# Kernel optimization log

Hardware: AMD Instinct MI355X
Metric: run time of the kernel (lower is better)

The kernel has to match this reference:

```python
import jax, jax.numpy as jnp
import numpy as np

N_NODES = 100_000
N_EDGES = 1_600_000
N_GRAPHS = 64
IN_CH = 128
HID = 64
OUT_CH = 2


def setup_inputs() -> dict:
    key = jax.random.key(0)
    ks = jax.random.split(key, 12)

    def lin(k, fan_in, fan_out):
        s = 1.0 / np.sqrt(fan_in)
        return jax.random.uniform(k, (fan_in, fan_out), jnp.float32, -s, s)

    x = jax.random.normal(ks[0], (N_NODES, IN_CH), jnp.float32)
    edge_index = jax.random.randint(ks[1], (2, N_EDGES), 0, N_NODES, jnp.int64)
    batch = jnp.sort(jax.random.randint(ks[2], (N_NODES,), 0, N_GRAPHS, jnp.int64))
    return {
        "x": x,
        "edge_index": edge_index,
        "batch": batch,
        "w_rel0": lin(ks[3], IN_CH, HID),
        "b_rel0": jnp.zeros((HID,), jnp.float32),
        "w_root0": lin(ks[4], IN_CH, HID),
        "w_rel1": lin(ks[5], HID, HID),
        "b_rel1": jnp.zeros((HID,), jnp.float32),
        "w_root1": lin(ks[6], HID, HID),
        "w_rel2": lin(ks[7], HID, HID),
        "b_rel2": jnp.zeros((HID,), jnp.float32),
        "w_root2": lin(ks[8], HID, HID),
        "head_w1": lin(ks[9], HID, HID),
        "head_b1": jnp.zeros((HID,), jnp.float32),
        "head_w2": lin(ks[10], HID, OUT_CH),
        "head_b2": jnp.zeros((OUT_CH,), jnp.float32),
    }


def _graph_conv(x, src, dst, w_rel, b_rel, w_root):
    # PyG GraphConv: out = lin_rel(sum_{j->i} x_j) + lin_root(x_i)
    agg = jax.ops.segment_sum(x[src], dst, num_segments=N_NODES)  # [N, d_in]
    return agg @ w_rel + b_rel + x @ w_root


def reference(x, edge_index, batch, w_rel0, b_rel0, w_root0,
              w_rel1, b_rel1, w_root1, w_rel2, b_rel2, w_root2,
              head_w1, head_b1, head_w2, head_b2):
    src, dst = edge_index[0], edge_index[1]
    h = jax.nn.relu(_graph_conv(x, src, dst, w_rel0, b_rel0, w_root0))
    h = jax.nn.relu(_graph_conv(h, src, dst, w_rel1, b_rel1, w_root1))
    h = jax.nn.relu(_graph_conv(h, src, dst, w_rel2, b_rel2, w_root2))
    # global_mean_pool over graph ids (dropout is identity at inference)
    sums = jax.ops.segment_sum(h, batch, num_segments=N_GRAPHS)          # [G, H]
    cnts = jax.ops.segment_sum(jnp.ones((N_NODES,), h.dtype), batch,
                               num_segments=N_GRAPHS)                    # [G]
    pooled = sums / jnp.maximum(cnts, 1.0)[:, None]
    z = jax.nn.relu(pooled @ head_w1 + head_b1)
    return z @ head_w2 + head_b2
```

## Files before the change

kernel.cpp:

```cpp
#include <hip/hip_runtime.h>
#include <hip/hip_bf16.h>

#define CAP 64
#define KBUCK 391
#define BSHIFT 8
#define BCAP 4608
#define CHUNK_A 2048
#define AITER (CHUNK_A / 256)
#define LDSZ 36864

typedef __attribute__((ext_vector_type(8))) short short8;
typedef __attribute__((ext_vector_type(4))) float f32x4;

__device__ inline unsigned short bfbits(float f) {
    __hip_bfloat16 b = __float2bfloat16(f);
    unsigned short u;
    __builtin_memcpy(&u, &b, 2);
    return u;
}

__device__ inline void bucket_body(char* smem, int bb, const int* __restrict__ ei,
                                   int E, int* __restrict__ gcur,
                                   unsigned* __restrict__ bucketed)
{
    int* hist = (int*)smem;
    int* base = hist + KBUCK;
    const int e0 = bb * CHUNK_A;
    const int e1 = min(e0 + CHUNK_A, E);
    for (int i = threadIdx.x; i < KBUCK; i += 256) hist[i] = 0;
    __syncthreads();
    int dreg[AITER];
    #pragma unroll
    for (int it = 0; it < AITER; ++it) {
        int e = e0 + it * 256 + threadIdx.x;
        dreg[it] = (e < e1) ? ei[E + e] : -1;
        if (dreg[it] >= 0) atomicAdd(&hist[dreg[it] >> BSHIFT], 1);
    }
    __syncthreads();
    for (int i = threadIdx.x; i < KBUCK; i += 256) {
        int h = hist[i];
        base[i] = h ? atomicAdd(&gcur[i], h) : 0;
        hist[i] = 0;
    }
    __syncthreads();
    #pragma unroll
    for (int it = 0; it < AITER; ++it) {
        int e = e0 + it * 256 + threadIdx.x;
        if (e < e1) {
            int s = ei[e];
            int d = dreg[it];
            int b = d >> BSHIFT;
            int off = base[b] + atomicAdd(&hist[b], 1);
            if (off < BCAP)
                bucketed[(size_t)b * BCAP + off] = ((unsigned)s << 8) | (unsigned)(d & 255);
        }
    }
}

__global__ __launch_bounds__(256) void build_slots_kernel(
    const unsigned* __restrict__ bucketed, const int* __restrict__ gcur,
    int* __restrict__ cnt, int* __restrict__ slots, int N)
{
    __shared__ int lcnt[256];
    const int b = blockIdx.x;
    const int nb0 = b << BSHIFT;
    lcnt[threadIdx.x] = 0;
    __syncthreads();
    const int count = min(gcur[b], BCAP);
    const unsigned* src = bucketed + (size_t)b * BCAP;
    for (int i = threadIdx.x; i < count; i += 256) {
        unsigned p = src[i];
        int dl = (int)(p & 255u);
        int pos = atomicAdd(&lcnt[dl], 1);
        if (pos < CAP) slots[(size_t)(nb0 + dl) * CAP + pos] = (int)(p >> 8);
    }
    __syncthreads();
    int node = nb0 + threadIdx.x;
    if (node < N) cnt[node] = min(lcnt[threadIdx.x], CAP);
}

__global__ __launch_bounds__(256) void prep_weights_kernel(
    const float* __restrict__ wr0, const float* __restrict__ wt0,
    const float* __restrict__ wr1, const float* __restrict__ wt1,
    const float* __restrict__ wr2, const float* __restrict__ wt2,
    __hip_bfloat16* __restrict__ hi, __hip_bfloat16* __restrict__ lo)
{
    int idx = blockIdx.x * 256 + threadIdx.x;
    if (idx >= 32768) return;
    const float *wr, *wt;
    int n, k;
    if (idx < 16384)      { wr = wr0; wt = wt0; int r = idx;         n = r >> 7; k = r & 127; }
    else if (idx < 24576) { wr = wr1; wt = wt1; int r = idx - 16384; n = r >> 6; k = r & 63; }
    else                  { wr = wr2; wt = wt2; int r = idx - 24576; n = r >> 6; k = r & 63; }
    float w = (n < 64) ? wr[k * 64 + n] : wt[k * 64 + (n - 64)];
    __hip_bfloat16 h = __float2bfloat16(w);
    hi[idx] = h;
    lo[idx] = __float2bfloat16(w - __bfloat162float(h));
}

template <int DIN, bool AFP32>
__device__ inline void mfma_body(
    char* smem, int bx, const void* __restrict__ featv,
    const __hip_bfloat16* __restrict__ whiT, const __hip_bfloat16* __restrict__ wloT,
    const float* __restrict__ b_rel,
    __hip_bfloat16* __restrict__ y, __hip_bfloat16* __restrict__ r, int N)
{
    __hip_bfloat16* As = (__hip_bfloat16*)smem;
    __hip_bfloat16* Bh = As + 128 * 48;
    __hip_bfloat16* Bl = Bh + 128 * 48;
    const int t = threadIdx.x;
    const int lane = t & 63;
    const int wid = t >> 6;
    const int wm = wid >> 1, wn = wid & 1;
    const int node0 = bx * 128;
    const int lrow = lane & 15;
    const int kgrp = lane >> 4;

    f32x4 acc[4][4];
    #pragma unroll
    for (int i = 0; i < 4; ++i)
        #pragma unroll
        for (int j = 0; j < 4; ++j) acc[i][j] = (f32x4){0.f, 0.f, 0.f, 0.f};

    for (int ks = 0; ks < DIN / 32; ++ks) {
        #pragma unroll
        for (int p = 0; p < 2; ++p) {
            int c = t + p * 256;
            int m = c >> 2, kc = c & 3;
            int row = node0 + m; if (row >= N) row = N - 1;
            if (AFP32) {
                const float* feat = (const float*)featv;
                const float* src = feat + (size_t)row * DIN + ks * 32 + kc * 8;
                float4 v0 = *(const float4*)src;
                float4 v1 = *(const float4*)(src + 4);
                union { uint4 q; unsigned short s[8]; } pk;
                pk.s[0] = bfbits(v0.x); pk.s[1] = bfbits(v0.y);
                pk.s[2] = bfbits(v0.z); pk.s[3] = bfbits(v0.w);
                pk.s[4] = bfbits(v1.x); pk.s[5] = bfbits(v1.y);
                pk.s[6] = bfbits(v1.z); pk.s[7] = bfbits(v1.w);
                *(uint4*)&As[m * 48 + kc * 8] = pk.q;
            } else {
                const __hip_bfloat16* feat = (const __hip_bfloat16*)featv;
                *(uint4*)&As[m * 48 + kc * 8] =
                    *(const uint4*)(feat + (size_t)row * DIN + ks * 32 + kc * 8);
            }
        }
        #pragma unroll
        for (int p = 0; p < 4; ++p) {
            int c = t + p * 256;
            int half = c >> 9;
            int cc = c & 511;
            int n = cc >> 2, kc = cc & 3;
            const __hip_bfloat16* w = half ? wloT : whiT;
            uint4 v = *(const uint4*)(w + (size_t)n * DIN + ks * 32 + kc * 8);
            if (half) *(uint4*)&Bl[n * 48 + kc * 8] = v;
            else      *(uint4*)&Bh[n * 48 + kc * 8] = v;
        }
        __syncthreads();

        short8 a[4], bh[4], bl[4];
        #pragma unroll
        for (int i = 0; i < 4; ++i)
            a[i] = *(const short8*)&As[(wm * 64 + i * 16 + lrow) * 48 + kgrp * 8];
        #pragma unroll
        for (int j = 0; j < 4; ++j) {
            bh[j] = *(const short8*)&Bh[(wn * 64 + j * 16 + lrow) * 48 + kgrp * 8];
            bl[j] = *(const short8*)&Bl[(wn * 64 + j * 16 + lrow) * 48 + kgrp * 8];
        }
        #pragma unroll
        for (int i = 0; i < 4; ++i)
            #pragma unroll
            for (int j = 0; j < 4; ++j) {
                acc[i][j] = __builtin_amdgcn_mfma_f32_16x16x32_bf16(a[i], bh[j], acc[i][j], 0, 0, 0);
                acc[i][j] = __builtin_amdgcn_mfma_f32_16x16x32_bf16(a[i], bl[j], acc[i][j], 0, 0, 0);
            }
        __syncthreads();
    }

    #pragma unroll
    for (int i = 0; i < 4; ++i) {
        int mbase = node0 + wm * 64 + i * 16 + kgrp * 4;
        #pragma unroll
        for (int j = 0; j < 4; ++j) {
            int n = wn * 64 + j * 16 + lrow;
            #pragma unroll
            for (int v = 0; v < 4; ++v) {
                int m = mbase + v;
                if (m < N) {
                    float val = acc[i][j][v];
                    if (n < 64) y[(size_t)m * 64 + n] = __float2bfloat16(val);
                    else        r[(size_t)m * 64 + (n - 64)] = __float2bfloat16(val + b_rel[n - 64]);
                }
            }
        }
    }
}

__global__ __launch_bounds__(256) void fused_l0_kernel(
    const float* __restrict__ x,
    const __hip_bfloat16* __restrict__ whiT, const __hip_bfloat16* __restrict__ wloT,
    const float* __restrict__ b_rel,
    __hip_bfloat16* __restrict__ y, __hip_bfloat16* __restrict__ r, int N,
    int gemm_blocks, const int* __restrict__ ei, int E,
    int* __restrict__ gcur, unsigned* __restrict__ bucketed)
{
    extern __shared__ char smem[];
    if ((int)blockIdx.x < gemm_blocks)
        mfma_body<128, true>(smem, blockIdx.x, x, whiT, wloT, b_rel, y, r, N);
    else
        bucket_body(smem, blockIdx.x - gemm_blocks, ei, E, gcur, bucketed);
}

template <int DIN>
__global__ __launch_bounds__(256) void mfma_lin_kernel(
    const __hip_bfloat16* __restrict__ feat,
    const __hip_bfloat16* __restrict__ whiT, const __hip_bfloat16* __restrict__ wloT,
    const float* __restrict__ b_rel,
    __hip_bfloat16* __restrict__ y, __hip_bfloat16* __restrict__ r, int N)
{
    extern __shared__ char smem[];
    mfma_body<DIN, false>(smem, blockIdx.x, feat, whiT, wloT, b_rel, y, r, N);
}

__global__ __launch_bounds__(256) void gather_relu_kernel(
    const __hip_bfloat16* __restrict__ y, const int* __restrict__ cnt,
    const int* __restrict__ slots, const __hip_bfloat16* __restrict__ rin,
    __hip_bfloat16* __restrict__ hout, int N)
{
    const int node = blockIdx.x * 8 + (threadIdx.x >> 5);
    if (node >= N) return;
    const int sub = threadIdx.x & 31;
    const int nb = sub >> 3;
    const int ch = (sub & 7) * 8;
    const int deg = cnt[node];
    const int* sl = slots + (size_t)node * CAP;
    const unsigned short* yp = (const unsigned short*)y;

    float a[8], b[8];
    #pragma unroll
    for (int k = 0; k < 8; ++k) { a[k] = 0.f; b[k] = 0.f; }

    #pragma unroll 2
    for (int j = nb; j < deg; j += 8) {
        int n0 = sl[j];
        uint4 v = *(const uint4*)(yp + (size_t)n0 * 64 + ch);
        a[0] += __uint_as_float(v.x << 16); a[1] += __uint_as_float(v.x & 0xffff0000u);
        a[2] += __uint_as_float(v.y << 16); a[3] += __uint_as_float(v.y & 0xffff0000u);
        a[4] += __uint_as_float(v.z << 16); a[5] += __uint_as_float(v.z & 0xffff0000u);
        a[6] += __uint_as_float(v.w << 16); a[7] += __uint_as_float(v.w & 0xffff0000u);
        int j2 = j + 4;
        if (j2 < deg) {
            int n1 = sl[j2];
            uint4 w = *(const uint4*)(yp + (size_t)n1 * 64 + ch);
            b[0] += __uint_as_float(w.x << 16); b[1] += __uint_as_float(w.x & 0xffff0000u);
            b[2] += __uint_as_float(w.y << 16); b[3] += __uint_as_float(w.y & 0xffff0000u);
            b[4] += __uint_as_float(w.z << 16); b[5] += __uint_as_float(w.z & 0xffff0000u);
            b[6] += __uint_as_float(w.w << 16); b[7] += __uint_as_float(w.w & 0xffff0000u);
        }
    }
    #pragma unroll
    for (int k = 0; k < 8; ++k) {
        a[k] += b[k];
        a[k] += __shfl_xor(a[k], 8);
        a[k] += __shfl_xor(a[k], 16);
    }
    if (nb == 0) {
        uint4 rv = *(const uint4*)((const unsigned short*)rin + (size_t)node * 64 + ch);
        float r0 = __uint_as_float(rv.x << 16), r1 = __uint_as_float(rv.x & 0xffff0000u);
        float r2 = __uint_as_float(rv.y << 16), r3 = __uint_as_float(rv.y & 0xffff0000u);
        float r4 = __uint_as_float(rv.z << 16), r5 = __uint_as_float(rv.z & 0xffff0000u);
        float r6 = __uint_as_float(rv.w << 16), r7 = __uint_as_float(rv.w & 0xffff0000u);
        float f0 = fmaxf(r0 + a[0], 0.f), f1 = fmaxf(r1 + a[1], 0.f);
        float f2 = fmaxf(r2 + a[2], 0.f), f3 = fmaxf(r3 + a[3], 0.f);
        float f4 = fmaxf(r4 + a[4], 0.f), f5 = fmaxf(r5 + a[5], 0.f);
        float f6 = fmaxf(r6 + a[6], 0.f), f7 = fmaxf(r7 + a[7], 0.f);
        union { uint4 q; unsigned short s[8]; } pk;
        pk.s[0] = bfbits(f0); pk.s[1] = bfbits(f1); pk.s[2] = bfbits(f2); pk.s[3] = bfbits(f3);
        pk.s[4] = bfbits(f4); pk.s[5] = bfbits(f5); pk.s[6] = bfbits(f6); pk.s[7] = bfbits(f7);
        *(uint4*)((unsigned short*)hout + (size_t)node * 64 + ch) = pk.q;
    }
}

__global__ __launch_bounds__(256) void pool_kernel(
    const __hip_bfloat16* __restrict__ h, const int* __restrict__ batch,
    float* __restrict__ gsum, int* __restrict__ gcnt, int N)
{
    const int CHUNK = 64;
    int wid = (blockIdx.x * 256 + threadIdx.x) >> 6;
    int lane = threadIdx.x & 63;
    int nb = lane >> 3;
    int ch = (lane & 7) * 8;
    int start = wid * CHUNK;
    if (start >= N) return;
    int end = min(start + CHUNK, N);
    const unsigned short* hp = (const unsigned short*)h;

    float a[8];
    #pragma unroll
    for (int k = 0; k < 8; ++k) a[k] = 0.f;
    int runcnt = 0;
    int i = start;
    int gcur = batch[start];

    while (i < end) {
        int idx = i + lane; if (idx > end - 1) idx = end - 1;
        int bl = batch[idx];
        unsigned long long diff = __ballot(bl != gcur && (i + lane) < end);
        int len = diff ? ((int)__ffsll(diff) - 1) : min(64, end - i);
        for (int j = i + nb; j < i + len; j += 8) {
            uint4 v = *(const uint4*)(hp + (size_t)j * 64 + ch);
            a[0] += __uint_as_float(v.x << 16); a[1] += __uint_as_float(v.x & 0xffff0000u);
            a[2] += __uint_as_float(v.y << 16); a[3] += __uint_as_float(v.y & 0xffff0000u);
            a[4] += __uint_as_float(v.z << 16); a[5] += __uint_as_float(v.z & 0xffff0000u);
            a[6] += __uint_as_float(v.w << 16); a[7] += __uint_as_float(v.w & 0xffff0000u);
        }
        runcnt += len;
        i += len;
        if (diff) {
            #pragma unroll
            for (int k = 0; k < 8; ++k) {
                a[k] += __shfl_xor(a[k], 8);
                a[k] += __shfl_xor(a[k], 16);
                a[k] += __shfl_xor(a[k], 32);
            }
            if (runcnt > 0) {
                if (nb == 0) {
                    #pragma unroll
                    for (int k = 0; k < 8; ++k)
                        atomicAdd(&gsum[gcur * 64 + ch + k], a[k]);
                }
                if (lane == 0) atomicAdd(&gcnt[gcur], runcnt);
            }
            #pragma unroll
            for (int k = 0; k < 8; ++k) a[k] = 0.f;
            runcnt = 0;
            gcur = __shfl(bl, len);
        }
    }
    #pragma unroll
    for (int k = 0; k < 8; ++k) {
        a[k] += __shfl_xor(a[k], 8);
        a[k] += __shfl_xor(a[k], 16);
        a[k] += __shfl_xor(a[k], 32);
    }
    if (runcnt > 0) {
        if (nb == 0) {
            #pragma unroll
            for (int k = 0; k < 8; ++k)
                atomicAdd(&gsum[gcur * 64 + ch + k], a[k]);
        }
        if (lane == 0) atomicAdd(&gcnt[gcur], runcnt);
    }
}

__global__ __launch_bounds__(256) void head_kernel(
    const float* __restrict__ gsum, const int* __restrict__ gcnt,
    const float* __restrict__ w1, const float* __restrict__ b1,
    const float* __restrict__ w2, const float* __restrict__ b2,
    float* __restrict__ out)
{
    __shared__ float pm[64 * 64];
    __shared__ float z[64 * 64];
    int t = threadIdx.x;
    for (int i = t; i < 64 * 64; i += 256) {
        int g = i >> 6;
        float cf = (float)gcnt[g];
        if (cf < 1.f) cf = 1.f;
        pm[i] = gsum[i] / cf;
    }
    __syncthreads();
    for (int i = t; i < 64 * 64; i += 256) {
        int g = i >> 6, c = i & 63;
        float a = b1[c];
        #pragma unroll 8
        for (int k = 0; k < 64; ++k) a = fmaf(pm[g * 64 + k], w1[k * 64 + c], a);
        z[i] = fmaxf(a, 0.f);
    }
    __syncthreads();
    for (int i = t; i < 64 * 2; i += 256) {
        int g = i >> 1, o = i & 1;
        float a = b2[o];
        #pragma unroll 8
        for (int k = 0; k < 64; ++k) a = fmaf(z[g * 64 + k], w2[k * 2 + o], a);
        out[i] = a;
    }
}

extern "C" void kernel_launch(void* const* d_in, const int* in_sizes, int n_in,
                              void* d_out, int out_size, void* d_ws, size_t ws_size,
                              hipStream_t stream)
{
    const float* x       = (const float*)d_in[0];
    const int*   ei      = (const int*)d_in[1];
    const int*   batch   = (const int*)d_in[2];
    const float* w_rel0  = (const float*)d_in[3];
    const float* b_rel0  = (const float*)d_in[4];
    const float* w_root0 = (const float*)d_in[5];
    const float* w_rel1  = (const float*)d_in[6];
    const float* b_rel1  = (const float*)d_in[7];
    const float* w_root1 = (const float*)d_in[8];
    const float* w_rel2  = (const float*)d_in[9];
    const float* b_rel2  = (const float*)d_in[10];
    const float* w_root2 = (const float*)d_in[11];
    const float* hw1     = (const float*)d_in[12];
    const float* hb1     = (const float*)d_in[13];
    const float* hw2     = (const float*)d_in[14];
    const float* hb2     = (const float*)d_in[15];
    float* out = (float*)d_out;

    const int N = in_sizes[0] / 128;
    const int E = in_sizes[1] / 2;
    const int G = 64;

    size_t off = 0;
    auto alloc = [&](size_t bytes) -> void* {
        void* p = (char*)d_ws + off;
        off += (bytes + 255) & ~(size_t)255;
        return p;
    };
    int*      cnt      = (int*)alloc((size_t)N * 4);
    int*      slots    = (int*)alloc((size_t)N * CAP * 4);
    unsigned* bucketed = (unsigned*)alloc((size_t)KBUCK * BCAP * 4);
    int*      gcur     = (int*)alloc((size_t)KBUCK * 4);
    __hip_bfloat16* whiT = (__hip_bfloat16*)alloc(32768 * 2);
    __hip_bfloat16* wloT = (__hip_bfloat16*)alloc(32768 * 2);
    __hip_bfloat16* ybf  = (__hip_bfloat16*)alloc((size_t)N * 64 * 2);
    __hip_bfloat16* h0   = (__hip_bfloat16*)alloc((size_t)N * 64 * 2);
    __hip_bfloat16* h1   = (__hip_bfloat16*)alloc((size_t)N * 64 * 2);
    __hip_bfloat16* rbf  = (__hip_bfloat16*)alloc((size_t)N * 64 * 2);
    float* gsum     = (float*)alloc((size_t)G * 64 * 4);
    int*   gcnt     = (int*)alloc((size_t)G * 4);
    (void)ws_size; (void)n_in;

    hipMemsetAsync(gcur, 0, (size_t)KBUCK * 4, stream);
    hipMemsetAsync(gsum, 0, (size_t)G * 64 * 4, stream);
    hipMemsetAsync(gcnt, 0, (size_t)G * 4, stream);

    prep_weights_kernel<<<128, 256, 0, stream>>>(w_rel0, w_root0, w_rel1, w_root1,
                                                 w_rel2, w_root2, whiT, wloT);

    const int gemm_blocks = (N + 127) / 128;
    const int bucket_blocks = (E + CHUNK_A - 1) / CHUNK_A;
    const int gather_blocks = (N + 7) / 8;

    fused_l0_kernel<<<gemm_blocks + bucket_blocks, 256, LDSZ, stream>>>(
        x, whiT, wloT, b_rel0, ybf, rbf, N, gemm_blocks, ei, E, gcur, bucketed);
    build_slots_kernel<<<KBUCK, 256, 0, stream>>>(bucketed, gcur, cnt, slots, N);
    gather_relu_kernel<<<gather_blocks, 256, 0, stream>>>(ybf, cnt, slots, rbf, h0, N);

    mfma_lin_kernel<64><<<gemm_blocks, 256, LDSZ, stream>>>(
        h0, whiT + 16384, wloT + 16384, b_rel1, ybf, rbf, N);
    gather_relu_kernel<<<gather_blocks, 256, 0, stream>>>(ybf, cnt, slots, rbf, h1, N);

    mfma_lin_kernel<64><<<gemm_blocks, 256, LDSZ, stream>>>(
        h1, whiT + 24576, wloT + 24576, b_rel2, ybf, rbf, N);
    gather_relu_kernel<<<gather_blocks, 256, 0, stream>>>(ybf, cnt, slots, rbf, h0, N);

    int pool_waves  = (N + 63) / 64;
    int pool_blocks = (pool_waves + 3) / 4;
    pool_kernel<<<pool_blocks, 256, 0, stream>>>(h0, batch, gsum, gcnt, N);
    head_kernel<<<1, 256, 0, stream>>>(gsum, gcnt, hw1, hb1, hw2, hb2, out);
}
```

Baseline: 376.0 us.

## Fuse neighbor gather with next-layer GEMM and pooling, drop lo-weight MFMA

Gather+ReLU is fused into the following layer's MFMA linear kernel through LDS, so the h0/h1 round trips to global memory and three kernel launches go away. The last gather is fused with mean pooling. Layers 1 and 2 now use only the bf16 high part of the weights, which halves MFMA work at some precision cost. Layer 0 overlays bucketing and the GEMM on the same blocks and shrinks LDS padding. Each GEMM block now runs 128 irregular gathers serially before its MFMA work, which may lower latency hiding.

```diff
diff --git a/kernel.cpp b/kernel.cpp
--- a/kernel.cpp
+++ b/kernel.cpp
@@ -7,13 +7,15 @@
 #define BCAP 4608
 #define CHUNK_A 2048
 #define AITER (CHUNK_A / 256)
-#define LDSZ 36864
+#define SA0 40
+#define SFG 72
 
 typedef __attribute__((ext_vector_type(8))) short short8;
 typedef __attribute__((ext_vector_type(4))) float f32x4;
+typedef __hip_bfloat16 bf16;
 
 __device__ inline unsigned short bfbits(float f) {
-    __hip_bfloat16 b = __float2bfloat16(f);
+    bf16 b = __float2bfloat16(f);
     unsigned short u;
     __builtin_memcpy(&u, &b, 2);
     return u;
@@ -57,57 +59,13 @@
     }
 }
 
-__global__ __launch_bounds__(256) void build_slots_kernel(
-    const unsigned* __restrict__ bucketed, const int* __restrict__ gcur,
-    int* __restrict__ cnt, int* __restrict__ slots, int N)
-{
-    __shared__ int lcnt[256];
-    const int b = blockIdx.x;
-    const int nb0 = b << BSHIFT;
-    lcnt[threadIdx.x] = 0;
-    __syncthreads();
-    const int count = min(gcur[b], BCAP);
-    const unsigned* src = bucketed + (size_t)b * BCAP;
-    for (int i = threadIdx.x; i < count; i += 256) {
-        unsigned p = src[i];
-        int dl = (int)(p & 255u);
-        int pos = atomicAdd(&lcnt[dl], 1);
-        if (pos < CAP) slots[(size_t)(nb0 + dl) * CAP + pos] = (int)(p >> 8);
-    }
-    __syncthreads();
-    int node = nb0 + threadIdx.x;
-    if (node < N) cnt[node] = min(lcnt[threadIdx.x], CAP);
-}
-
-__global__ __launch_bounds__(256) void prep_weights_kernel(
-    const float* __restrict__ wr0, const float* __restrict__ wt0,
-    const float* __restrict__ wr1, const float* __restrict__ wt1,
-    const float* __restrict__ wr2, const float* __restrict__ wt2,
-    __hip_bfloat16* __restrict__ hi, __hip_bfloat16* __restrict__ lo)
-{
-    int idx = blockIdx.x * 256 + threadIdx.x;
-    if (idx >= 32768) return;
-    const float *wr, *wt;
-    int n, k;
-    if (idx < 16384)      { wr = wr0; wt = wt0; int r = idx;         n = r >> 7; k = r & 127; }
-    else if (idx < 24576) { wr = wr1; wt = wt1; int r = idx - 16384; n = r >> 6; k = r & 63; }
-    else                  { wr = wr2; wt = wt2; int r = idx - 24576; n = r >> 6; k = r & 63; }
-    float w = (n < 64) ? wr[k * 64 + n] : wt[k * 64 + (n - 64)];
-    __hip_bfloat16 h = __float2bfloat16(w);
-    hi[idx] = h;
-    lo[idx] = __float2bfloat16(w - __bfloat162float(h));
-}
-
-template <int DIN, bool AFP32>
-__device__ inline void mfma_body(
-    char* smem, int bx, const void* __restrict__ featv,
-    const __hip_bfloat16* __restrict__ whiT, const __hip_bfloat16* __restrict__ wloT,
-    const float* __restrict__ b_rel,
-    __hip_bfloat16* __restrict__ y, __hip_bfloat16* __restrict__ r, int N)
-{
-    __hip_bfloat16* As = (__hip_bfloat16*)smem;
-    __hip_bfloat16* Bh = As + 128 * 48;
-    __hip_bfloat16* Bl = Bh + 128 * 48;
+__device__ inline void lin0_body(char* smem, int bx, const float* __restrict__ x,
+    const bf16* __restrict__ whiT, const bf16* __restrict__ wloT,
+    const float* __restrict__ b_rel, bf16* __restrict__ y, bf16* __restrict__ r, int N)
+{
+    bf16* As = (bf16*)smem;
+    bf16* Bh = As + 128 * SA0;
+    bf16* Bl = Bh + 128 * SA0;
     const int t = threadIdx.x;
     const int lane = t & 63;
     const int wid = t >> 6;
@@ -122,28 +80,21 @@
         #pragma unroll
         for (int j = 0; j < 4; ++j) acc[i][j] = (f32x4){0.f, 0.f, 0.f, 0.f};
 
-    for (int ks = 0; ks < DIN / 32; ++ks) {
+    for (int ks = 0; ks < 4; ++ks) {
         #pragma unroll
         for (int p = 0; p < 2; ++p) {
             int c = t + p * 256;
             int m = c >> 2, kc = c & 3;
             int row = node0 + m; if (row >= N) row = N - 1;
-            if (AFP32) {
-                const float* feat = (const float*)featv;
-                const float* src = feat + (size_t)row * DIN + ks * 32 + kc * 8;
-                float4 v0 = *(const float4*)src;
-                float4 v1 = *(const float4*)(src + 4);
-                union { uint4 q; unsigned short s[8]; } pk;
-                pk.s[0] = bfbits(v0.x); pk.s[1] = bfbits(v0.y);
-                pk.s[2] = bfbits(v0.z); pk.s[3] = bfbits(v0.w);
-                pk.s[4] = bfbits(v1.x); pk.s[5] = bfbits(v1.y);
-                pk.s[6] = bfbits(v1.z); pk.s[7] = bfbits(v1.w);
-                *(uint4*)&As[m * 48 + kc * 8] = pk.q;
-            } else {
-                const __hip_bfloat16* feat = (const __hip_bfloat16*)featv;
-                *(uint4*)&As[m * 48 + kc * 8] =
-                    *(const uint4*)(feat + (size_t)row * DIN + ks * 32 + kc * 8);
-            }
+            const float* src = x + (size_t)row * 128 + ks * 32 + kc * 8;
+            float4 v0 = *(const float4*)src;
+            float4 v1 = *(const float4*)(src + 4);
+            union { uint4 q; unsigned short s[8]; } pk;
+            pk.s[0] = bfbits(v0.x); pk.s[1] = bfbits(v0.y);
+            pk.s[2] = bfbits(v0.z); pk.s[3] = bfbits(v0.w);
+            pk.s[4] = bfbits(v1.x); pk.s[5] = bfbits(v1.y);
+            pk.s[6] = bfbits(v1.z); pk.s[7] = bfbits(v1.w);
+            *(uint4*)&As[m * SA0 + kc * 8] = pk.q;
         }
         #pragma unroll
         for (int p = 0; p < 4; ++p) {
@@ -151,21 +102,21 @@
             int half = c >> 9;
             int cc = c & 511;
             int n = cc >> 2, kc = cc & 3;
-            const __hip_bfloat16* w = half ? wloT : whiT;
-            uint4 v = *(const uint4*)(w + (size_t)n * DIN + ks * 32 + kc * 8);
-            if (half) *(uint4*)&Bl[n * 48 + kc * 8] = v;
-            else      *(uint4*)&Bh[n * 48 + kc * 8] = v;
+            const bf16* w = half ? wloT : whiT;
+            uint4 v = *(const uint4*)(w + (size_t)n * 128 + ks * 32 + kc * 8);
+            if (half) *(uint4*)&Bl[n * SA0 + kc * 8] = v;
+            else      *(uint4*)&Bh[n * SA0 + kc * 8] = v;
         }
         __syncthreads();
 
         short8 a[4], bh[4], bl[4];
         #pragma unroll
         for (int i = 0; i < 4; ++i)
-            a[i] = *(const short8*)&As[(wm * 64 + i * 16 + lrow) * 48 + kgrp * 8];
+            a[i] = *(const short8*)&As[(wm * 64 + i * 16 + lrow) * SA0 + kgrp * 8];
         #pragma unroll
         for (int j = 0; j < 4; ++j) {
-            bh[j] = *(const short8*)&Bh[(wn * 64 + j * 16 + lrow) * 48 + kgrp * 8];
-            bl[j] = *(const short8*)&Bl[(wn * 64 + j * 16 + lrow) * 48 + kgrp * 8];
+            bh[j] = *(const short8*)&Bh[(wn * 64 + j * 16 + lrow) * SA0 + kgrp * 8];
+            bl[j] = *(const short8*)&Bl[(wn * 64 + j * 16 + lrow) * SA0 + kgrp * 8];
         }
         #pragma unroll
         for (int i = 0; i < 4; ++i)
@@ -198,159 +149,226 @@
 
 __global__ __launch_bounds__(256) void fused_l0_kernel(
     const float* __restrict__ x,
-    const __hip_bfloat16* __restrict__ whiT, const __hip_bfloat16* __restrict__ wloT,
+    const bf16* __restrict__ whiT, const bf16* __restrict__ wloT,
     const float* __restrict__ b_rel,
-    __hip_bfloat16* __restrict__ y, __hip_bfloat16* __restrict__ r, int N,
-    int gemm_blocks, const int* __restrict__ ei, int E,
-    int* __restrict__ gcur, unsigned* __restrict__ bucketed)
+    bf16* __restrict__ y, bf16* __restrict__ r, int N,
+    const int* __restrict__ ei, int E,
+    int* __restrict__ gcur, unsigned* __restrict__ bucketed,
+    int bucket_blocks, int gemm_blocks)
 {
     extern __shared__ char smem[];
+    if ((int)blockIdx.x < bucket_blocks)
+        bucket_body(smem, blockIdx.x, ei, E, gcur, bucketed);
+    __syncthreads();
     if ((int)blockIdx.x < gemm_blocks)
-        mfma_body<128, true>(smem, blockIdx.x, x, whiT, wloT, b_rel, y, r, N);
-    else
-        bucket_body(smem, blockIdx.x - gemm_blocks, ei, E, gcur, bucketed);
-}
-
-template <int DIN>
-__global__ __launch_bounds__(256) void mfma_lin_kernel(
-    const __hip_bfloat16* __restrict__ feat,
-    const __hip_bfloat16* __restrict__ whiT, const __hip_bfloat16* __restrict__ wloT,
-    const float* __restrict__ b_rel,
-    __hip_bfloat16* __restrict__ y, __hip_bfloat16* __restrict__ r, int N)
-{
-    extern __shared__ char smem[];
-    mfma_body<DIN, false>(smem, blockIdx.x, feat, whiT, wloT, b_rel, y, r, N);
-}
-
-__global__ __launch_bounds__(256) void gather_relu_kernel(
-    const __hip_bfloat16* __restrict__ y, const int* __restrict__ cnt,
-    const int* __restrict__ slots, const __hip_bfloat16* __restrict__ rin,
-    __hip_bfloat16* __restrict__ hout, int N)
-{
-    const int node = blockIdx.x * 8 + (threadIdx.x >> 5);
-    if (node >= N) return;
+        lin0_body(smem, blockIdx.x, x, whiT, wloT, b_rel, y, r, N);
+}
+
+__global__ __launch_bounds__(256) void build_slots_kernel(
+    const unsigned* __restrict__ bucketed, const int* __restrict__ gcur,
+    int* __restrict__ cnt, int* __restrict__ slots, int N)
+{
+    __shared__ int lcnt[256];
+    const int b = blockIdx.x;
+    const int nb0 = b << BSHIFT;
+    lcnt[threadIdx.x] = 0;
+    __syncthreads();
+    const int count = min(gcur[b], BCAP);
+    const unsigned* src = bucketed + (size_t)b * BCAP;
+    for (int i = threadIdx.x; i < count; i += 256) {
+        unsigned p = src[i];
+        int dl = (int)(p & 255u);
+        int pos = atomicAdd(&lcnt[dl], 1);
+        if (pos < CAP) slots[(size_t)(nb0 + dl) * CAP + pos] = (int)(p >> 8);
+    }
+    __syncthreads();
+    int node = nb0 + threadIdx.x;
+    if (node < N) cnt[node] = min(lcnt[threadIdx.x], CAP);
+}
+
+__global__ __launch_bounds__(256) void prep_weights_kernel(
+    const float* __restrict__ wr0, const float* __restrict__ wt0,
+    const float* __restrict__ wr1, const float* __restrict__ wt1,
+    const float* __restrict__ wr2, const float* __restrict__ wt2,
+    bf16* __restrict__ hi, bf16* __restrict__ lo)
+{
+    int idx = blockIdx.x * 256 + threadIdx.x;
+    if (idx >= 32768) return;
+    const float *wr, *wt;
+    int n, k;
+    if (idx < 16384)      { wr = wr0; wt = wt0; int q = idx;         n = q >> 7; k = q & 127; }
+    else if (idx < 24576) { wr = wr1; wt = wt1; int q = idx - 16384; n = q >> 6; k = q & 63; }
+    else                  { wr = wr2; wt = wt2; int q = idx - 24576; n = q >> 6; k = q & 63; }
+    float w = (n < 64) ? wr[k * 64 + n] : wt[k * 64 + (n - 64)];
+    bf16 h = __float2bfloat16(w);
+    hi[idx] = h;
+    lo[idx] = __float2bfloat16(w - __bfloat162float(h));
+}
+
+__device__ inline void gather_to_lds(bf16* As, int node0,
+    const bf16* __restrict__ y, const int* __restrict__ cnt,
+    const int* __restrict__ slots, const bf16* __restrict__ rin, int N)
+{
     const int sub = threadIdx.x & 31;
     const int nb = sub >> 3;
     const int ch = (sub & 7) * 8;
-    const int deg = cnt[node];
-    const int* sl = slots + (size_t)node * CAP;
     const unsigned short* yp = (const unsigned short*)y;
 
-    float a[8], b[8];
-    #pragma unroll
-    for (int k = 0; k < 8; ++k) { a[k] = 0.f; b[k] = 0.f; }
-
-    #pragma unroll 2
-    for (int j = nb; j < deg; j += 8) {
-        int n0 = sl[j];
-        uint4 v = *(const uint4*)(yp + (size_t)n0 * 64 + ch);
-        a[0] += __uint_as_float(v.x << 16); a[1] += __uint_as_float(v.x & 0xffff0000u);
-        a[2] += __uint_as_float(v.y << 16); a[3] += __uint_as_float(v.y & 0xffff0000u);
-        a[4] += __uint_as_float(v.z << 16); a[5] += __uint_as_float(v.z & 0xffff0000u);
-        a[6] += __uint_as_float(v.w << 16); a[7] += __uint_as_float(v.w & 0xffff0000u);
-        int j2 = j + 4;
-        if (j2 < deg) {
-            int n1 = sl[j2];
-            uint4 w = *(const uint4*)(yp + (size_t)n1 * 64 + ch);
-            b[0] += __uint_as_float(w.x << 16); b[1] += __uint_as_float(w.x & 0xffff0000u);
-            b[2] += __uint_as_float(w.y << 16); b[3] += __uint_as_float(w.y & 0xffff0000u);
-            b[4] += __uint_as_float(w.z << 16); b[5] += __uint_as_float(w.z & 0xffff0000u);
-            b[6] += __uint_as_float(w.w << 16); b[7] += __uint_as_float(w.w & 0xffff0000u);
-        }
-    }
-    #pragma unroll
-    for (int k = 0; k < 8; ++k) {
-        a[k] += b[k];
-        a[k] += __shfl_xor(a[k], 8);
-        a[k] += __shfl_xor(a[k], 16);
-    }
-    if (nb == 0) {
-        uint4 rv = *(const uint4*)((const unsigned short*)rin + (size_t)node * 64 + ch);
-        float r0 = __uint_as_float(rv.x << 16), r1 = __uint_as_float(rv.x & 0xffff0000u);
-        float r2 = __uint_as_float(rv.y << 16), r3 = __uint_as_float(rv.y & 0xffff0000u);
-        float r4 = __uint_as_float(rv.z << 16), r5 = __uint_as_float(rv.z & 0xffff0000u);
-        float r6 = __uint_as_float(rv.w << 16), r7 = __uint_as_float(rv.w & 0xffff0000u);
-        float f0 = fmaxf(r0 + a[0], 0.f), f1 = fmaxf(r1 + a[1], 0.f);
-        float f2 = fmaxf(r2 + a[2], 0.f), f3 = fmaxf(r3 + a[3], 0.f);
-        float f4 = fmaxf(r4 + a[4], 0.f), f5 = fmaxf(r5 + a[5], 0.f);
-        float f6 = fmaxf(r6 + a[6], 0.f), f7 = fmaxf(r7 + a[7], 0.f);
-        union { uint4 q; unsigned short s[8]; } pk;
-        pk.s[0] = bfbits(f0); pk.s[1] = bfbits(f1); pk.s[2] = bfbits(f2); pk.s[3] = bfbits(f3);
-        pk.s[4] = bfbits(f4); pk.s[5] = bfbits(f5); pk.s[6] = bfbits(f6); pk.s[7] = bfbits(f7);
-        *(uint4*)((unsigned short*)hout + (size_t)node * 64 + ch) = pk.q;
-    }
-}
-
-__global__ __launch_bounds__(256) void pool_kernel(
-    const __hip_bfloat16* __restrict__ h, const int* __restrict__ batch,
-    float* __restrict__ gsum, int* __restrict__ gcnt, int N)
-{
-    const int CHUNK = 64;
-    int wid = (blockIdx.x * 256 + threadIdx.x) >> 6;
-    int lane = threadIdx.x & 63;
-    int nb = lane >> 3;
-    int ch = (lane & 7) * 8;
-    int start = wid * CHUNK;
-    if (start >= N) return;
-    int end = min(start + CHUNK, N);
-    const unsigned short* hp = (const unsigned short*)h;
-
-    float a[8];
-    #pragma unroll
-    for (int k = 0; k < 8; ++k) a[k] = 0.f;
-    int runcnt = 0;
-    int i = start;
-    int gcur = batch[start];
-
-    while (i < end) {
-        int idx = i + lane; if (idx > end - 1) idx = end - 1;
-        int bl = batch[idx];
-        unsigned long long diff = __ballot(bl != gcur && (i + lane) < end);
-        int len = diff ? ((int)__ffsll(diff) - 1) : min(64, end - i);
-        for (int j = i + nb; j < i + len; j += 8) {
-            uint4 v = *(const uint4*)(hp + (size_t)j * 64 + ch);
+    for (int p = 0; p < 16; ++p) {
+        int nl = p * 8 + (threadIdx.x >> 5);
+        int node = node0 + nl; if (node >= N) node = N - 1;
+        const int deg = cnt[node];
+        const int* sl = slots + (size_t)node * CAP;
+
+        float a[8], b[8];
+        #pragma unroll
+        for (int k = 0; k < 8; ++k) { a[k] = 0.f; b[k] = 0.f; }
+
+        #pragma unroll 2
+        for (int j = nb; j < deg; j += 8) {
+            int n0 = sl[j];
+            uint4 v = *(const uint4*)(yp + (size_t)n0 * 64 + ch);
             a[0] += __uint_as_float(v.x << 16); a[1] += __uint_as_float(v.x & 0xffff0000u);
             a[2] += __uint_as_float(v.y << 16); a[3] += __uint_as_float(v.y & 0xffff0000u);
             a[4] += __uint_as_float(v.z << 16); a[5] += __uint_as_float(v.z & 0xffff0000u);
             a[6] += __uint_as_float(v.w << 16); a[7] += __uint_as_float(v.w & 0xffff0000u);
-        }
-        runcnt += len;
-        i += len;
-        if (diff) {
+            int j2 = j + 4;
+            if (j2 < deg) {
+                int n1 = sl[j2];
+                uint4 w = *(const uint4*)(yp + (size_t)n1 * 64 + ch);
+                b[0] += __uint_as_float(w.x << 16); b[1] += __uint_as_float(w.x & 0xffff0000u);
+                b[2] += __uint_as_float(w.y << 16); b[3] += __uint_as_float(w.y & 0xffff0000u);
+                b[4] += __uint_as_float(w.z << 16); b[5] += __uint_as_float(w.z & 0xffff0000u);
+                b[6] += __uint_as_float(w.w << 16); b[7] += __uint_as_float(w.w & 0xffff0000u);
+            }
+        }
+        #pragma unroll
+        for (int k = 0; k < 8; ++k) {
+            a[k] += b[k];
+            a[k] += __shfl_xor(a[k], 8);
+            a[k] += __shfl_xor(a[k], 16);
+        }
+        if (nb == 0) {
+            uint4 rv = *(const uint4*)((const unsigned short*)rin + (size_t)node * 64 + ch);
+            float r0 = __uint_as_float(rv.x << 16), r1 = __uint_as_float(rv.x & 0xffff0000u);
+            float r2 = __uint_as_float(rv.y << 16), r3 = __uint_as_float(rv.y & 0xffff0000u);
+            float r4 = __uint_as_float(rv.z << 16), r5 = __uint_as_float(rv.z & 0xffff0000u);
+            float r6 = __uint_as_float(rv.w << 16), r7 = __uint_as_float(rv.w & 0xffff0000u);
+            union { uint4 q; unsigned short s[8]; } pk;
+            pk.s[0] = bfbits(fmaxf(r0 + a[0], 0.f)); pk.s[1] = bfbits(fmaxf(r1 + a[1], 0.f));
+            pk.s[2] = bfbits(fmaxf(r2 + a[2], 0.f)); pk.s[3] = bfbits(fmaxf(r3 + a[3], 0.f));
+            pk.s[4] = bfbits(fmaxf(r4 + a[4], 0.f)); pk.s[5] = bfbits(fmaxf(r5 + a[5], 0.f));
+            pk.s[6] = bfbits(fmaxf(r6 + a[6], 0.f)); pk.s[7] = bfbits(fmaxf(r7 + a[7], 0.f));
+            *(uint4*)&As[nl * SFG + ch] = pk.q;
+        }
+    }
+}
+
+__global__ __launch_bounds__(256) void fg_lin_kernel(
+    const bf16* __restrict__ yin, const int* __restrict__ cnt,
+    const int* __restrict__ slots, const bf16* __restrict__ rin,
+    const bf16* __restrict__ whiT, const float* __restrict__ b_rel,
+    bf16* __restrict__ yout, bf16* __restrict__ rout, int N)
+{
+    extern __shared__ char smem[];
+    bf16* As = (bf16*)smem;
+    bf16* Bs = As + 128 * SFG;
+    const int node0 = blockIdx.x * 128;
+
+    gather_to_lds(As, node0, yin, cnt, slots, rin, N);
+
+    const int t = threadIdx.x;
+    const int lane = t & 63;
+    const int wid = t >> 6;
+    const int wm = wid >> 1, wn = wid & 1;
+    const int lrow = lane & 15;
+    const int kgrp = lane >> 4;
+
+    f32x4 acc[4][4];
+    #pragma unroll
+    for (int i = 0; i < 4; ++i)
+        #pragma unroll
+        for (int j = 0; j < 4; ++j) acc[i][j] = (f32x4){0.f, 0.f, 0.f, 0.f};
+
+    for (int ks = 0; ks < 2; ++ks) {
+        __syncthreads();
+        #pragma unroll
+        for (int p = 0; p < 2; ++p) {
+            int c = t + p * 256;
+            int n = c >> 2, kc = c & 3;
+            *(uint4*)&Bs[n * SA0 + kc * 8] =
+                *(const uint4*)(whiT + (size_t)n * 64 + ks * 32 + kc * 8);
+        }
+        __syncthreads();
+
+        short8 a[4], b[4];
+        #pragma unroll
+        for (int i = 0; i < 4; ++i)
+            a[i] = *(const short8*)&As[(wm * 64 + i * 16 + lrow) * SFG + ks * 32 + kgrp * 8];
+        #pragma unroll
+        for (int j = 0; j < 4; ++j)
+            b[j] = *(const short8*)&Bs[(wn * 64 + j * 16 + lrow) * SA0 + kgrp * 8];
+        #pragma unroll
+        for (int i = 0; i < 4; ++i)
             #pragma unroll
-            for (int k = 0; k < 8; ++k) {
-                a[k] += __shfl_xor(a[k], 8);
-                a[k] += __shfl_xor(a[k], 16);
-                a[k] += __shfl_xor(a[k], 32);
+            for (int j = 0; j < 4; ++j)
+                acc[i][j] = __builtin_amdgcn_mfma_f32_16x16x32_bf16(a[i], b[j], acc[i][j], 0, 0, 0);
+    }
+
+    #pragma unroll
+    for (int i = 0; i < 4; ++i) {
+        int mbase = node0 + wm * 64 + i * 16 + kgrp * 4;
+        #pragma unroll
+        for (int j = 0; j < 4; ++j) {
+            int n = wn * 64 + j * 16 + lrow;
+            #pragma unroll
+            for (int v = 0; v < 4; ++v) {
+                int m = mbase + v;
+                if (m < N) {
+                    float val = acc[i][j][v];
+                    if (n < 64) yout[(size_t)m * 64 + n] = __float2bfloat16(val);
+                    else        rout[(size_t)m * 64 + (n - 64)] = __float2bfloat16(val + b_rel[n - 64]);
+                }
             }
-            if (runcnt > 0) {
-                if (nb == 0) {
-                    #pragma unroll
-                    for (int k = 0; k < 8; ++k)
-                        atomicAdd(&gsum[gcur * 64 + ch + k], a[k]);
-                }
-                if (lane == 0) atomicAdd(&gcnt[gcur], runcnt);
-            }
-            #pragma unroll
-            for (int k = 0; k < 8; ++k) a[k] = 0.f;
-            runcnt = 0;
-            gcur = __shfl(bl, len);
-        }
-    }
-    #pragma unroll
-    for (int k = 0; k < 8; ++k) {
-        a[k] += __shfl_xor(a[k], 8);
-        a[k] += __shfl_xor(a[k], 16);
-        a[k] += __shfl_xor(a[k], 32);
-    }
-    if (runcnt > 0) {
-        if (nb == 0) {
-            #pragma unroll
-            for (int k = 0; k < 8; ++k)
-                atomicAdd(&gsum[gcur * 64 + ch + k], a[k]);
-        }
-        if (lane == 0) atomicAdd(&gcnt[gcur], runcnt);
-    }
+        }
+    }
+}
+
+__global__ __launch_bounds__(256) void fg_pool_kernel(
+    const bf16* __restrict__ yin, const int* __restrict__ cnt,
+    const int* __restrict__ slots, const bf16* __restrict__ rin,
+    const int* __restrict__ batch, float* __restrict__ gsum,
+    int* __restrict__ gcnt, int N)
+{
+    extern __shared__ char smem[];
+    bf16* As = (bf16*)smem;
+    const int node0 = blockIdx.x * 128;
+
+    gather_to_lds(As, node0, yin, cnt, slots, rin, N);
+    __syncthreads();
+
+    const int wid = threadIdx.x >> 6;
+    const int lane = threadIdx.x & 63;
+    int rbeg = wid * 32;
+    int rlim = N - node0; if (rlim > 128) rlim = 128;
+    int rend = rbeg + 32; if (rend > rlim) rend = rlim;
+    if (rbeg >= rend) return;
+
+    int g = batch[node0 + rbeg];
+    float acc = 0.f;
+    int run = 0;
+    for (int i = rbeg; i < rend; ++i) {
+        int gg = batch[node0 + i];
+        if (gg != g) {
+            atomicAdd(&gsum[g * 64 + lane], acc);
+            if (lane == 0) atomicAdd(&gcnt[g], run);
+            acc = 0.f; run = 0; g = gg;
+        }
+        acc += __bfloat162float(As[i * SFG + lane]);
+        ++run;
+    }
+    atomicAdd(&gsum[g * 64 + lane], acc);
+    if (lane == 0) atomicAdd(&gcnt[g], run);
 }
 
 __global__ __launch_bounds__(256) void head_kernel(
@@ -422,14 +440,14 @@
     int*      slots    = (int*)alloc((size_t)N * CAP * 4);
     unsigned* bucketed = (unsigned*)alloc((size_t)KBUCK * BCAP * 4);
     int*      gcur     = (int*)alloc((size_t)KBUCK * 4);
-    __hip_bfloat16* whiT = (__hip_bfloat16*)alloc(32768 * 2);
-    __hip_bfloat16* wloT = (__hip_bfloat16*)alloc(32768 * 2);
-    __hip_bfloat16* ybf  = (__hip_bfloat16*)alloc((size_t)N * 64 * 2);
-    __hip_bfloat16* h0   = (__hip_bfloat16*)alloc((size_t)N * 64 * 2);
-    __hip_bfloat16* h1   = (__hip_bfloat16*)alloc((size_t)N * 64 * 2);
-    __hip_bfloat16* rbf  = (__hip_bfloat16*)alloc((size_t)N * 64 * 2);
-    float* gsum     = (float*)alloc((size_t)G * 64 * 4);
-    int*   gcnt     = (int*)alloc((size_t)G * 4);
+    bf16* whiT = (bf16*)alloc(32768 * 2);
+    bf16* wloT = (bf16*)alloc(32768 * 2);
+    bf16* yA   = (bf16*)alloc((size_t)N * 64 * 2);
+    bf16* rA   = (bf16*)alloc((size_t)N * 64 * 2);
+    bf16* yB   = (bf16*)alloc((size_t)N * 64 * 2);
+    bf16* rB   = (bf16*)alloc((size_t)N * 64 * 2);
+    float* gsum = (float*)alloc((size_t)G * 64 * 4);
+    int*   gcnt = (int*)alloc((size_t)G * 4);
     (void)ws_size; (void)n_in;
 
     hipMemsetAsync(gcur, 0, (size_t)KBUCK * 4, stream);
@@ -439,25 +457,24 @@
     prep_weights_kernel<<<128, 256, 0, stream>>>(w_rel0, w_root0, w_rel1, w_root1,
                                                  w_rel2, w_root2, whiT, wloT);
 
-    const int gemm_blocks = (N + 127) / 128;
+    const int gemm_blocks   = (N + 127) / 128;
     const int bucket_blocks = (E + CHUNK_A - 1) / CHUNK_A;
-    const int gather_blocks = (N + 7) / 8;
-
-    fused_l0_kernel<<<gemm_blocks + bucket_blocks, 256, LDSZ, stream>>>(
-        x, whiT, wloT, b_rel0, ybf, rbf, N, gemm_blocks, ei, E, gcur, bucketed);
+    const int grid = max(gemm_blocks, bucket_blocks);
+    const size_t LDS_L0 = (size_t)3 * 128 * SA0 * 2;
+    const size_t LDS_FG = (size_t)128 * SFG * 2 + (size_t)128 * SA0 * 2;
+    const size_t LDS_FP = (size_t)128 * SFG * 2;
+
+    fused_l0_kernel<<<grid, 256, LDS_L0, stream>>>(
+        x, whiT, wloT, b_rel0, yA, rA, N, ei, E, gcur, bucketed,
+        bucket_blocks, gemm_blocks);
     build_slots_kernel<<<KBUCK, 256, 0, stream>>>(bucketed, gcur, cnt, slots, N);
-    gather_relu_kernel<<<gather_blocks, 256, 0, stream>>>(ybf, cnt, slots, rbf, h0, N);
-
-    mfma_lin_kernel<64><<<gemm_blocks, 256, LDSZ, stream>>>(
-        h0, whiT + 16384, wloT + 16384, b_rel1, ybf, rbf, N);
-    gather_relu_kernel<<<gather_blocks, 256, 0, stream>>>(ybf, cnt, slots, rbf, h1, N);
-
-    mfma_lin_kernel<64><<<gemm_blocks, 256, LDSZ, stream>>>(
-        h1, whiT + 24576, wloT + 24576, b_rel2, ybf, rbf, N);
-    gather_relu_kernel<<<gather_blocks, 256, 0, stream>>>(ybf, cnt, slots, rbf, h0, N);
-
-    int pool_waves  = (N + 63) / 64;
-    int pool_blocks = (pool_waves + 3) / 4;
-    pool_kernel<<<pool_blocks, 256, 0, stream>>>(h0, batch, gsum, gcnt, N);
+
+    fg_lin_kernel<<<gemm_blocks, 256, LDS_FG, stream>>>(
+        yA, cnt, slots, rA, whiT + 16384, b_rel1, yB, rB, N);
+    fg_lin_kernel<<<gemm_blocks, 256, LDS_FG, stream>>>(
+        yB, cnt, slots, rB, whiT + 24576, b_rel2, yA, rA, N);
+    fg_pool_kernel<<<gemm_blocks, 256, LDS_FP, stream>>>(
+        yA, cnt, slots, rA, batch, gsum, gcnt, N);
+
     head_kernel<<<1, 256, 0, stream>>>(gsum, gcnt, hw1, hb1, hw2, hb2, out);
 }
```

New measurement: 576.1 us. +53.2%, slower.
